# Optimization experiments

Measured on AMD Instinct MI355X. Metric: run time of the kernel, lower is better.

The kernel has to match this reference:

```python
import jax, jax.numpy as jnp
import numpy as np

RADIUS = 6
KSIZE = 2 * RADIUS + 1  # 13


def setup_inputs() -> dict:
    key = jax.random.key(0)
    k1, k2 = jax.random.split(key)
    B, C, H, W = 8, 256, 128, 128
    z_t = jax.random.normal(k1, (B, C, H, W), dtype=jnp.float32)
    z_t1 = jax.random.normal(k2, (B, C, H, W), dtype=jnp.float32)
    return {"z_t": z_t, "z_t1": z_t1}


def reference(z_t, z_t1):
    B, C, H, W = z_t.shape
    r, K = RADIUS, KSIZE
    # zero-pad neighbor frame spatially (matches F.unfold padding=radius)
    zp = jnp.pad(z_t1, ((0, 0), (0, 0), (r, r), (r, r)))
    # kernel tap offsets in torch-unfold order: index k = i*K + j (row-major)
    ii, jj = jnp.meshgrid(jnp.arange(K), jnp.arange(K), indexing="ij")
    offsets = jnp.stack([ii.reshape(-1), jj.reshape(-1)], axis=-1)  # [K*K, 2]

    def tap(carry, off):
        # window: padded[:, :, i:i+H, j:j+W]  == z_t1 shifted by (i-r, j-r)
        win = jax.lax.dynamic_slice(zp, (0, 0, off[0], off[1]), (B, C, H, W))
        s = jnp.einsum("bchw,bchw->bhw", z_t, win)  # channel dot per pixel
        return carry, s

    _, scores = jax.lax.scan(tap, None, offsets)  # [K*K, B, H, W]
    scores = jnp.transpose(scores, (1, 0, 2, 3))  # [B, K*K, H, W]
    return scores / jnp.sqrt(jnp.asarray(C, dtype=z_t.dtype))
```

## Files before the change

### kernel.cpp

```cpp
#include <hip/hip_runtime.h>
#include <hip/hip_bf16.h>


#define CC 256
#define HH 128
#define WW 128
#define NT 169
#define PH 8
#define PW 16
#define QH 20
#define QW 28
#define CCH 32
#define NCH 8
#define CS 40
#define NPIXB (QH*QW)
#define NPIXA (PH*PW)
#define NUB (NPIXB*4)
#define NUNIT (NUB + NPIXA*4)
#define UPT 6
#define CHPLANE (HH*WW)
#define ABYTE (NPIXB*CS*2)
#define KHALF 85
#define OSTRIDE 132

typedef __attribute__((ext_vector_type(8))) short bf16x8;
typedef __attribute__((ext_vector_type(4))) float f32x4;

union SMEM {
    unsigned short stage[NPIXB*CS + NPIXA*CS];
    float outb[KHALF*OSTRIDE];
};

static __device__ __forceinline__ unsigned pk2(float a, float b) {
    unsigned x = __bfloat16_as_ushort(__float2bfloat16(a));
    unsigned y = __bfloat16_as_ushort(__float2bfloat16(b));
    return x | (y << 16);
}

__global__ __launch_bounds__(512, 2)
void lc_mfma(const float* __restrict__ zt, const float* __restrict__ zt1,
             float* __restrict__ out) {
    __shared__ SMEM sm;
    char* smb = (char*)&sm;

    const int tid  = threadIdx.x;
    const int lane = tid & 63;
    const int wid  = tid >> 6;
    const int py0  = (wid >> 2) * 4;
    const int px0  = (wid & 3) * 4;

    const int bid = blockIdx.x;
    const int b   = bid & 7;
    const int t   = bid >> 3;
    const int h0  = (t >> 3) * PH;
    const int w0  = (t & 7) * PW;

    const float* src[UPT];
    int   dstB[UPT];
    bool  ex[UPT], pv[UPT];
#pragma unroll
    for (int v = 0; v < UPT; ++v) {
        const int ui = tid + v * 512;
        ex[v] = ui < NUNIT;
        int pix, oct, gy, gx, valid;
        const float* base;
        if (ui < NUB) {
            oct = ui / NPIXB;
            pix = ui - oct * NPIXB;
            const int qyi = pix / QW;
            const int qxi = pix - qyi * QW;
            gy = h0 + qyi - 6;
            gx = w0 + qxi - 6;
            valid = (gy >= 0) & (gy < HH) & (gx >= 0) & (gx < WW);
            base = zt1;
            dstB[v] = pix * (CS*2) + oct * 16;
        } else {
            const int u2 = ui - NUB;
            oct = u2 >> 7;
            pix = u2 & 127;
            gy = h0 + (pix >> 4);
            gx = w0 + (pix & 15);
            valid = 1;
            base = zt;
            dstB[v] = ABYTE + pix * (CS*2) + oct * 16;
        }
        pv[v] = valid;
        src[v] = base + (((b * CC + oct * 8) * HH + (valid ? gy : 0)) * WW + (valid ? gx : 0));
    }

    const int nlo = lane & 3, nhi = (lane >> 2) & 3, oo = lane >> 4;
    int boff[16];
#pragma unroll
    for (int qi = 0; qi < 16; ++qi) {
        const int qyL = py0 + (qi >> 2) * 4 + nhi;
        const int qxL = px0 + (qi & 3) * 4 + nlo;
        boff[qi] = (qyL * QW + qxL) * (CS*2) + oo * 16;
    }
    const int pixA = (py0 + nhi) * PW + px0 + nlo;
    const int aoff = ABYTE + pixA * (CS*2) + oo * 16;

    f32x4 acc[16];
#pragma unroll
    for (int qi = 0; qi < 16; ++qi) acc[qi] = (f32x4){0.f, 0.f, 0.f, 0.f};

    float pf[UPT][8];
#pragma unroll
    for (int v = 0; v < UPT; ++v) {
        const bool ld = ex[v] && pv[v];
#pragma unroll
        for (int j = 0; j < 8; ++j) pf[v][j] = ld ? src[v][j * CHPLANE] : 0.f;
        src[v] += CCH * CHPLANE;
    }

    for (int kc = 0; kc < NCH; ++kc) {
#pragma unroll
        for (int v = 0; v < UPT; ++v) {
            if (ex[v]) {
                uint4 q;
                q.x = pk2(pf[v][0], pf[v][1]);
                q.y = pk2(pf[v][2], pf[v][3]);
                q.z = pk2(pf[v][4], pf[v][5]);
                q.w = pk2(pf[v][6], pf[v][7]);
                *(uint4*)(smb + dstB[v]) = q;
            }
        }
        if (kc + 1 < NCH) {
#pragma unroll
            for (int v = 0; v < UPT; ++v) {
                const bool ld = ex[v] && pv[v];
#pragma unroll
                for (int j = 0; j < 8; ++j) pf[v][j] = ld ? src[v][j * CHPLANE] : 0.f;
                src[v] += CCH * CHPLANE;
            }
        }
        __syncthreads();

        const bf16x8 af = *(const bf16x8*)(smb + aoff);
#pragma unroll
        for (int qi = 0; qi < 16; ++qi) {
            const bf16x8 bfr = *(const bf16x8*)(smb + boff[qi]);
            acc[qi] = __builtin_amdgcn_mfma_f32_16x16x32_bf16(af, bfr, acc[qi], 0, 0, 0);
        }
        __syncthreads();
    }

    const int psb = (py0 + oo) * PW + px0;
#pragma unroll 1
    for (int pass = 0; pass < 2; ++pass) {
        const int kb = pass * KHALF;
        const int nk = pass ? (NT - KHALF) : KHALF;
#pragma unroll
        for (int qi = 0; qi < 16; ++qi) {
            const int di = 4 * (qi >> 2) + nhi - oo;
            const bool diok = (unsigned)di <= 12u;
            const int dib = di * 13;
#pragma unroll
            for (int r = 0; r < 4; ++r) {
                const int dj = 4 * (qi & 3) + nlo - r;
                const int k  = dib + dj;
                if (diok && (unsigned)dj <= 12u && k >= kb && k < kb + nk)
                    sm.outb[(k - kb) * OSTRIDE + psb + r] = acc[qi][r] * 0.0625f;
            }
        }
        __syncthreads();
        const int total4 = nk * 32;
        for (int i = tid; i < total4; i += 512) {
            const int row = i >> 5, j = i & 31;
            const float4 val = *(const float4*)&sm.outb[row * OSTRIDE + j * 4];
            float* dst = out + (((b * NT + kb + row) * HH + h0 + (j >> 2)) * WW
                                + w0 + (j & 3) * 4);
            *(float4*)dst = val;
        }
        __syncthreads();
    }
}

extern "C" void kernel_launch(void* const* d_in, const int* in_sizes, int n_in,
                              void* d_out, int out_size, void* d_ws, size_t ws_size,
                              hipStream_t stream) {
    const float* zt  = (const float*)d_in[0];
    const float* zt1 = (const float*)d_in[1];
    float* out = (float*)d_out;
    lc_mfma<<<dim3(1024), dim3(512), 0, stream>>>(zt, zt1, out);
}
```

Measured before the change: 143.5 us.

## Rewrite correlation kernel with async global-to-LDS pipeline and 1024-thread blocks

Replaces the register-staged load path with direct global_load_lds of raw fp32 rows into a four-slot LDS ring, then converts to bf16 fragments in LDS with an XOR swizzle. A operands are now held in registers for all 256 channels, and blocks grow to 1024 threads, with each wave computing half of the neighbour tiles. Out-of-range loads read from a zeroed workspace buffer set by an extra tiny kernel, and sync is done with hand-written waitcnt and barrier asm. The goal is to overlap global loads with compute and cut register traffic. The cost is more LDS (about 150 KB per block, so likely one block per CU), lower occupancy, and an extra kernel launch.

New measurement: 215.8 us. +50.3%, slower.

```diff
diff --git a/kernel.cpp b/kernel.cpp
--- a/kernel.cpp
+++ b/kernel.cpp
@@ -2,155 +2,159 @@
 #include <hip/hip_bf16.h>
 
 
-#define CC 256
 #define HH 128
 #define WW 128
+#define CCT 256
 #define NT 169
-#define PH 8
 #define PW 16
-#define QH 20
 #define QW 28
-#define CCH 32
-#define NCH 8
-#define CS 40
-#define NPIXB (QH*QW)
-#define NPIXA (PH*PW)
-#define NUB (NPIXB*4)
-#define NUNIT (NUB + NPIXA*4)
-#define UPT 6
-#define CHPLANE (HH*WW)
-#define ABYTE (NPIXB*CS*2)
 #define KHALF 85
 #define OSTRIDE 132
+#define RAWQ 20480
+#define FRAGOFF 81920
+#define FRAGSZ 35840
+#define SMTOT (FRAGOFF + 2*FRAGSZ)
+#define CHPL (HH*WW)
 
 typedef __attribute__((ext_vector_type(8))) short bf16x8;
 typedef __attribute__((ext_vector_type(4))) float f32x4;
 
-union SMEM {
-    unsigned short stage[NPIXB*CS + NPIXA*CS];
-    float outb[KHALF*OSTRIDE];
-};
+union SMEM { char raw[SMTOT]; float outb[KHALF*OSTRIDE]; };
 
 static __device__ __forceinline__ unsigned pk2(float a, float b) {
-    unsigned x = __bfloat16_as_ushort(__float2bfloat16(a));
-    unsigned y = __bfloat16_as_ushort(__float2bfloat16(b));
-    return x | (y << 16);
+    __hip_bfloat162 h = __float22bfloat162_rn(make_float2(a, b));
+    union { __hip_bfloat162 h2; unsigned u; } c; c.h2 = h; return c.u;
 }
 
-__global__ __launch_bounds__(512, 2)
-void lc_mfma(const float* __restrict__ zt, const float* __restrict__ zt1,
-             float* __restrict__ out) {
+__global__ void zero_ws(float* w) { if (threadIdx.x < 256) w[threadIdx.x] = 0.f; }
+
+__global__ __launch_bounds__(1024)
+void lc5(const float* __restrict__ zt, const float* __restrict__ zt1,
+         const float* __restrict__ zpg, float* __restrict__ out) {
     __shared__ SMEM sm;
-    char* smb = (char*)&sm;
+    char* smb = sm.raw;
+    const int tid = threadIdx.x, lane = tid & 63, wid = tid >> 6;
+    const int bid = blockIdx.x;
+    const int b = bid & 7, t = bid >> 3;
+    const int h0 = (t >> 3) * 8, w0 = (t & 7) * PW;
 
-    const int tid  = threadIdx.x;
-    const int lane = tid & 63;
-    const int wid  = tid >> 6;
-    const int py0  = (wid >> 2) * 4;
-    const int px0  = (wid & 3) * 4;
+    const int pw = wid & 7, qh = wid >> 3;
+    const int py0 = (pw >> 2) * 4, px0w = (pw & 3) * 4;
+    const int nlo = lane & 3, nhi = (lane >> 2) & 3, oo = lane >> 4;
 
-    const int bid = blockIdx.x;
-    const int b   = bid & 7;
-    const int t   = bid >> 3;
-    const int h0  = (t >> 3) * PH;
-    const int w0  = (t & 7) * PW;
-
-    const float* src[UPT];
-    int   dstB[UPT];
-    bool  ex[UPT], pv[UPT];
-#pragma unroll
-    for (int v = 0; v < UPT; ++v) {
-        const int ui = tid + v * 512;
-        ex[v] = ui < NUNIT;
-        int pix, oct, gy, gx, valid;
-        const float* base;
-        if (ui < NUB) {
-            oct = ui / NPIXB;
-            pix = ui - oct * NPIXB;
-            const int qyi = pix / QW;
-            const int qxi = pix - qyi * QW;
-            gy = h0 + qyi - 6;
-            gx = w0 + qxi - 6;
-            valid = (gy >= 0) & (gy < HH) & (gx >= 0) & (gx < WW);
-            base = zt1;
-            dstB[v] = pix * (CS*2) + oct * 16;
-        } else {
-            const int u2 = ui - NUB;
-            oct = u2 >> 7;
-            pix = u2 & 127;
-            gy = h0 + (pix >> 4);
-            gx = w0 + (pix & 15);
-            valid = 1;
-            base = zt;
-            dstB[v] = ABYTE + pix * (CS*2) + oct * 16;
-        }
-        pv[v] = valid;
-        src[v] = base + (((b * CC + oct * 8) * HH + (valid ? gy : 0)) * WW + (valid ? gx : 0));
+    const float* gp0; const float* gp1; int gadv0, gadv1;
+    {
+        const int u = wid * 64 + lane;
+        const int part = u & 7, tt = u >> 3;
+        const int ch = tt / 20, qy = tt - ch * 20;
+        const int gy = h0 + qy - 6, gxs = w0 - 8 + part * 4;
+        const bool val = (gy >= 0) && (gy < HH) && (gxs >= 0) && (gxs <= WW - 4);
+        gp0 = val ? zt1 + (((size_t)(b * CCT + ch) * HH + gy) * WW + gxs)
+                  : zpg + (u & 63) * 4;
+        gadv0 = val ? 8 * CHPL : 0;
+    }
+    {
+        const int u = 1024 + wid * 16 + (lane & 15);
+        const int part = u & 7, tt = u >> 3;
+        const int ch = tt / 20, qy = tt - ch * 20;
+        const int gy = h0 + qy - 6, gxs = w0 - 8 + part * 4;
+        const bool val = (gy >= 0) && (gy < HH) && (gxs >= 0) && (gxs <= WW - 4);
+        gp1 = val ? zt1 + (((size_t)(b * CCT + ch) * HH + gy) * WW + gxs)
+                  : zpg + (u & 63) * 4;
+        gadv1 = val ? 8 * CHPL : 0;
     }
 
-    const int nlo = lane & 3, nhi = (lane >> 2) & 3, oo = lane >> 4;
-    int boff[16];
-#pragma unroll
-    for (int qi = 0; qi < 16; ++qi) {
-        const int qyL = py0 + (qi >> 2) * 4 + nhi;
-        const int qxL = px0 + (qi & 3) * 4 + nlo;
-        boff[qi] = (qyL * QW + qxL) * (CS*2) + oo * 16;
-    }
-    const int pixA = (py0 + nhi) * PW + px0 + nlo;
-    const int aoff = ABYTE + pixA * (CS*2) + oo * 16;
-
-    f32x4 acc[16];
-#pragma unroll
-    for (int qi = 0; qi < 16; ++qi) acc[qi] = (f32x4){0.f, 0.f, 0.f, 0.f};
-
-    float pf[UPT][8];
-#pragma unroll
-    for (int v = 0; v < UPT; ++v) {
-        const bool ld = ex[v] && pv[v];
-#pragma unroll
-        for (int j = 0; j < 8; ++j) pf[v][j] = ld ? src[v][j * CHPLANE] : 0.f;
-        src[v] += CCH * CHPLANE;
+    int rbyte = 0, fwb = 0, fxor = 0;
+    if (tid < 560) {
+        const int pqy = tid / 28, pqx = tid - pqy * 28;
+        rbyte = (pqy * 32 + pqx + 2) * 4;
+        fwb = FRAGOFF + tid * 64;
+        fxor = (pqx + pqy) & 3;
     }
 
-    for (int kc = 0; kc < NCH; ++kc) {
+    int boff[8];
 #pragma unroll
-        for (int v = 0; v < UPT; ++v) {
-            if (ex[v]) {
-                uint4 q;
-                q.x = pk2(pf[v][0], pf[v][1]);
-                q.y = pk2(pf[v][2], pf[v][3]);
-                q.z = pk2(pf[v][4], pf[v][5]);
-                q.w = pk2(pf[v][6], pf[v][7]);
-                *(uint4*)(smb + dstB[v]) = q;
+    for (int jj = 0; jj < 8; ++jj) {
+        const int qi = qh * 8 + jj;
+        const int qyL = py0 + (qi >> 2) * 4 + nhi;
+        const int qxL = px0w + (qi & 3) * 4 + nlo;
+        boff[jj] = FRAGOFF + (qyL * QW + qxL) * 64 + ((oo ^ ((qxL + qyL) & 3)) << 4);
+    }
+
+    bf16x8 abf[8];
+    {
+        const float* ap = zt + (((size_t)(b * CCT + oo * 8) * HH + (h0 + py0 + nhi)) * WW
+                                + (w0 + px0w + nlo));
+#pragma unroll
+        for (int pr = 0; pr < 8; ++pr) {
+            float a8[8];
+#pragma unroll
+            for (int e = 0; e < 8; ++e) a8[e] = ap[(size_t)(pr * 32 + e) * CHPL];
+            union { unsigned u[4]; bf16x8 v; } au;
+            au.u[0] = pk2(a8[0], a8[1]); au.u[1] = pk2(a8[2], a8[3]);
+            au.u[2] = pk2(a8[4], a8[5]); au.u[3] = pk2(a8[6], a8[7]);
+            abf[pr] = au.v;
+        }
+    }
+
+#define GISSUE(SLOT) do {                                                      \
+    __builtin_amdgcn_global_load_lds(                                          \
+        (const __attribute__((address_space(1))) void*)gp0,                    \
+        (__attribute__((address_space(3))) void*)(smb + (SLOT) * RAWQ + wid * 1024), \
+        16, 0, 0);                                                             \
+    gp0 += gadv0;                                                              \
+    if (lane < 16)                                                             \
+        __builtin_amdgcn_global_load_lds(                                      \
+            (const __attribute__((address_space(1))) void*)gp1,                \
+            (__attribute__((address_space(3))) void*)(smb + (SLOT) * RAWQ + 16384 + wid * 256), \
+            16, 0, 0);                                                         \
+    gp1 += gadv1;                                                              \
+} while (0)
+
+    f32x4 acc[8];
+#pragma unroll
+    for (int j = 0; j < 8; ++j) acc[j] = (f32x4){0.f, 0.f, 0.f, 0.f};
+
+    GISSUE(0); GISSUE(1); GISSUE(2);
+
+#pragma unroll
+    for (int pr = 0; pr < 8; ++pr) {
+#pragma unroll
+        for (int sub = 0; sub < 4; ++sub) {
+            const int q = 4 * pr + sub;
+            if (q < 30)       asm volatile("s_waitcnt vmcnt(4)\n\ts_barrier" ::: "memory");
+            else if (q == 30) asm volatile("s_waitcnt vmcnt(2)\n\ts_barrier" ::: "memory");
+            else              asm volatile("s_waitcnt vmcnt(0)\n\ts_barrier" ::: "memory");
+            if (q + 3 < 32) { GISSUE((q + 3) & 3); }
+            if (tid < 560) {
+                const char* rb = smb + (q & 3) * RAWQ + rbyte;
+                float f[8];
+#pragma unroll
+                for (int e = 0; e < 8; ++e) f[e] = *(const float*)(rb + e * 2560);
+                uint4 qq;
+                qq.x = pk2(f[0], f[1]); qq.y = pk2(f[2], f[3]);
+                qq.z = pk2(f[4], f[5]); qq.w = pk2(f[6], f[7]);
+                *(uint4*)(smb + ((q >> 2) & 1) * FRAGSZ + fwb + ((sub ^ fxor) << 4)) = qq;
             }
         }
-        if (kc + 1 < NCH) {
+        asm volatile("s_waitcnt lgkmcnt(0)\n\ts_barrier" ::: "memory");
+        const int P = (pr & 1) * FRAGSZ;
 #pragma unroll
-            for (int v = 0; v < UPT; ++v) {
-                const bool ld = ex[v] && pv[v];
-#pragma unroll
-                for (int j = 0; j < 8; ++j) pf[v][j] = ld ? src[v][j * CHPLANE] : 0.f;
-                src[v] += CCH * CHPLANE;
-            }
+        for (int jj = 0; jj < 8; ++jj) {
+            const bf16x8 bfr = *(const bf16x8*)(smb + P + boff[jj]);
+            acc[jj] = __builtin_amdgcn_mfma_f32_16x16x32_bf16(abf[pr], bfr, acc[jj], 0, 0, 0);
         }
-        __syncthreads();
-
-        const bf16x8 af = *(const bf16x8*)(smb + aoff);
-#pragma unroll
-        for (int qi = 0; qi < 16; ++qi) {
-            const bf16x8 bfr = *(const bf16x8*)(smb + boff[qi]);
-            acc[qi] = __builtin_amdgcn_mfma_f32_16x16x32_bf16(af, bfr, acc[qi], 0, 0, 0);
-        }
-        __syncthreads();
     }
 
-    const int psb = (py0 + oo) * PW + px0;
+    const int psb = (py0 + oo) * PW + px0w;
 #pragma unroll 1
     for (int pass = 0; pass < 2; ++pass) {
         const int kb = pass * KHALF;
         const int nk = pass ? (NT - KHALF) : KHALF;
+        __syncthreads();
 #pragma unroll
-        for (int qi = 0; qi < 16; ++qi) {
+        for (int jj = 0; jj < 8; ++jj) {
+            const int qi = qh * 8 + jj;
             const int di = 4 * (qi >> 2) + nhi - oo;
             const bool diok = (unsigned)di <= 12u;
             const int dib = di * 13;
@@ -159,19 +163,18 @@
                 const int dj = 4 * (qi & 3) + nlo - r;
                 const int k  = dib + dj;
                 if (diok && (unsigned)dj <= 12u && k >= kb && k < kb + nk)
-                    sm.outb[(k - kb) * OSTRIDE + psb + r] = acc[qi][r] * 0.0625f;
+                    sm.outb[(k - kb) * OSTRIDE + psb + r] = acc[jj][r] * 0.0625f;
             }
         }
         __syncthreads();
         const int total4 = nk * 32;
-        for (int i = tid; i < total4; i += 512) {
+        for (int i = tid; i < total4; i += 1024) {
             const int row = i >> 5, j = i & 31;
             const float4 val = *(const float4*)&sm.outb[row * OSTRIDE + j * 4];
-            float* dst = out + (((b * NT + kb + row) * HH + h0 + (j >> 2)) * WW
+            float* dst = out + (((size_t)(b * NT + kb + row) * HH + h0 + (j >> 2)) * WW
                                 + w0 + (j & 3) * 4);
             *(float4*)dst = val;
         }
-        __syncthreads();
     }
 }
 
@@ -181,5 +184,7 @@
     const float* zt  = (const float*)d_in[0];
     const float* zt1 = (const float*)d_in[1];
     float* out = (float*)d_out;
-    lc_mfma<<<dim3(1024), dim3(512), 0, stream>>>(zt, zt1, out);
+    float* ws  = (float*)d_ws;
+    zero_ws<<<dim3(1), dim3(256), 0, stream>>>(ws);
+    lc5<<<dim3(1024), dim3(1024), 0, stream>>>(zt, zt1, (const float*)ws, out);
 }
```
